# Performance work log

Hardware: AMD Instinct MI355X
Metric: run time of the kernel (lower is better)

## Reference

```python
import jax, jax.numpy as jnp
import numpy as np

B, C, H, W = 16, 64, 128, 128
HX, HY = 64, 64


def _rnn_scan(x, Wih, Whh, bih, bhh):
    """Vanilla tanh RNN, batch_first. x: [N, T, Cin] -> [N, T, Hh]."""
    # precompute input projection with one big GEMM
    pre = jnp.einsum('ntc,hc->nth', x, Wih) + bih + bhh  # [N,T,Hh]
    N = x.shape[0]
    h0 = jnp.zeros((N, Whh.shape[0]), dtype=x.dtype)

    def step(h, p):
        h = jnp.tanh(p + h @ Whh.T)
        return h, h

    _, ys = jax.lax.scan(step, h0, jnp.swapaxes(pre, 0, 1))  # [T,N,Hh]
    return jnp.swapaxes(ys, 0, 1)


def setup_inputs() -> dict:
    key = jax.random.key(0)
    ks = jax.random.split(key, 9)
    sx = 1.0 / np.sqrt(HX)
    sy = 1.0 / np.sqrt(HY)
    return {
        'x': jax.random.normal(ks[0], (B, C, H, W), dtype=jnp.float32),
        'Wih_x': jax.random.uniform(ks[1], (HX, C), jnp.float32, -sx, sx),
        'Whh_x': jax.random.uniform(ks[2], (HX, HX), jnp.float32, -sx, sx),
        'bih_x': jax.random.uniform(ks[3], (HX,), jnp.float32, -sx, sx),
        'bhh_x': jax.random.uniform(ks[4], (HX,), jnp.float32, -sx, sx),
        'Wih_y': jax.random.uniform(ks[5], (HY, HX), jnp.float32, -sy, sy),
        'Whh_y': jax.random.uniform(ks[6], (HY, HY), jnp.float32, -sy, sy),
        'bih_y': jax.random.uniform(ks[7], (HY,), jnp.float32, -sy, sy),
        'bhh_y': jax.random.uniform(ks[8], (HY,), jnp.float32, -sy, sy),
    }


def reference(x, Wih_x, Whh_x, bih_x, bhh_x, Wih_y, Whh_y, bih_y, bhh_y):
    b, c, h, w = x.shape
    # X-axis RNN: scan along width, sequences are rows
    xw = jnp.transpose(x, (0, 2, 3, 1)).reshape(b * h, w, c)  # [B*H, W, C]
    out_x = _rnn_scan(xw, Wih_x, Whh_x, bih_x, bhh_x)          # [B*H, W, HX]
    # Y-axis RNN: scan along height, sequences are columns
    xy = out_x.reshape(b, h, w, HX)
    xy = jnp.transpose(xy, (0, 2, 1, 3)).reshape(b * w, h, HX)  # [B*W, H, HX]
    out_y = _rnn_scan(xy, Wih_y, Whh_y, bih_y, bhh_y)           # [B*W, H, HY]
    out = out_y.reshape(b, w, h, HY)
    return jnp.transpose(out, (0, 3, 2, 1))  # [B, HY, H, W]
```

## Files before the change

### kernel.cpp

```cpp
#include <hip/hip_runtime.h>
#include <stdint.h>


#define TLEN 128
#define NSEQ 2048
#define PSH (NSEQ*64)
#define GT 16

typedef __bf16   bf16x8 __attribute__((ext_vector_type(8)));
typedef _Float16 f16x4  __attribute__((ext_vector_type(4)));
typedef float    f32x4  __attribute__((ext_vector_type(4)));
typedef unsigned short u16x4 __attribute__((ext_vector_type(4)));

static __device__ __forceinline__ unsigned int fbits(float f){
    union { float f; unsigned int u; } v; v.f = f; return v.u;
}
static __device__ __forceinline__ float ubits(unsigned int u){
    union { unsigned int u; float f; } v; v.u = u; return v.f;
}
static __device__ __forceinline__ float bf2f(unsigned short s){ return ubits(((unsigned int)s) << 16); }
static __device__ __forceinline__ unsigned short f2bf(float f){
    unsigned int u = fbits(f);
    return (unsigned short)((u + 0x7FFFu + ((u >> 16) & 1u)) >> 16);
}
static __device__ __forceinline__ __bf16 us2b(unsigned short s){
    union { unsigned short u; __bf16 b; } v; v.u = s; return v.b;
}
struct bfpair { __bf16 hi, lo; };
static __device__ __forceinline__ bfpair splitf(float f){
    unsigned short h = f2bf(f);
    bfpair r; r.hi = us2b(h); r.lo = us2b(f2bf(f - bf2f(h))); return r;
}
static __device__ __forceinline__ float fast_tanh(float x){
    float e = __builtin_amdgcn_exp2f(x * 2.8853900817779268f);
    return 1.0f - 2.0f * __builtin_amdgcn_rcpf(e + 1.0f);
}

__global__ __launch_bounds__(256) void k_proj0(const float* __restrict__ A,
                                               const float* __restrict__ Wih,
                                               const float* __restrict__ b1,
                                               const float* __restrict__ b2,
                                               _Float16* __restrict__ pre){
    int lane = threadIdx.x & 63;
    int wv   = threadIdx.x >> 6;
    int q    = lane >> 4, l15 = lane & 15;

    bf16x8 Whi[4][2], Wlo[4][2];
#pragma unroll
    for (int n = 0; n < 4; n++)
#pragma unroll
        for (int kc = 0; kc < 2; kc++){
            const float* p = Wih + (n * 16 + l15) * 64 + kc * 32 + q * 8;
#pragma unroll
            for (int i = 0; i < 8; i++){
                bfpair s = splitf(p[i]);
                Whi[n][kc][i] = s.hi; Wlo[n][kc][i] = s.lo;
            }
        }
    float bias[4];
#pragma unroll
    for (int n = 0; n < 4; n++){
        int j = n * 16 + l15;
        bias[n] = b1[j] + b2[j];
    }

    int row0 = blockIdx.x * 128 + wv * 32;

    float av[2][2][8];
#pragma unroll
    for (int mi = 0; mi < 2; mi++){
        int r = row0 + mi * 16 + l15;
        int b = r >> 14, hw = r & 16383;
        const float* xb = A + (size_t)b * 1048576 + hw;
#pragma unroll
        for (int kc = 0; kc < 2; kc++)
#pragma unroll
            for (int i = 0; i < 8; i++)
                av[mi][kc][i] = xb[(size_t)(kc * 32 + q * 8 + i) * 16384];
    }

#pragma unroll
    for (int mi = 0; mi < 2; mi++){
        int rb = row0 + mi * 16;
        bf16x8 Ahi[2], Alo[2];
#pragma unroll
        for (int kc = 0; kc < 2; kc++)
#pragma unroll
            for (int i = 0; i < 8; i++){
                bfpair s = splitf(av[mi][kc][i]);
                Ahi[kc][i] = s.hi; Alo[kc][i] = s.lo;
            }
        f32x4 acc[4];
#pragma unroll
        for (int n = 0; n < 4; n++) acc[n] = (f32x4){bias[n], bias[n], bias[n], bias[n]};
#pragma unroll
        for (int n = 0; n < 4; n++)
#pragma unroll
            for (int kc = 0; kc < 2; kc++){
                acc[n] = __builtin_amdgcn_mfma_f32_16x16x32_bf16(Ahi[kc], Whi[n][kc], acc[n], 0, 0, 0);
                acc[n] = __builtin_amdgcn_mfma_f32_16x16x32_bf16(Alo[kc], Whi[n][kc], acc[n], 0, 0, 0);
                acc[n] = __builtin_amdgcn_mfma_f32_16x16x32_bf16(Ahi[kc], Wlo[n][kc], acc[n], 0, 0, 0);
            }
        int bT = rb >> 14, hT = (rb >> 7) & 127, wBase = rb & 127;
        size_t seqOff = (size_t)bT * 128 + hT;
#pragma unroll
        for (int n = 0; n < 4; n++)
#pragma unroll
            for (int rr = 0; rr < 4; rr++){
                int w = wBase + q * 4 + rr;
                pre[((size_t)w * NSEQ + seqOff) * 64 + n * 16 + l15] = (_Float16)acc[n][rr];
            }
    }
}

template<int PASS>
__global__ __launch_bounds__(256) void k_scan(const _Float16* __restrict__ pre,
                                              const float* __restrict__ Whh,
                                              const float* __restrict__ Wy,
                                              const float* __restrict__ by1,
                                              const float* __restrict__ by2,
                                              _Float16* __restrict__ prey,
                                              float* __restrict__ outf){
    __shared__ alignas(16) unsigned short hbuf[2][2][16][64];
    int lane = threadIdx.x & 63;
    int wv   = threadIdx.x >> 6;
    int q = lane >> 4, l15 = lane & 15;
    int n0 = blockIdx.x * 16;
    int j0 = wv * 16 + q * 4;

    bf16x8 Ahi[2], Alo[2];
#pragma unroll
    for (int kc = 0; kc < 2; kc++){
        const float* p = Whh + (wv * 16 + l15) * 64 + kc * 32 + q * 8;
#pragma unroll
        for (int i = 0; i < 8; i++){
            bfpair s = splitf(p[i]);
            Ahi[kc][i] = s.hi; Alo[kc][i] = s.lo;
        }
    }
    bf16x8 Yhi[2], Ylo[2];
    f32x4  biasy = (f32x4){0.f, 0.f, 0.f, 0.f};
    if constexpr (PASS == 0){
#pragma unroll
        for (int kc = 0; kc < 2; kc++){
            const float* p = Wy + (wv * 16 + l15) * 64 + kc * 32 + q * 8;
#pragma unroll
            for (int i = 0; i < 8; i++){
                bfpair s = splitf(p[i]);
                Yhi[kc][i] = s.hi; Ylo[kc][i] = s.lo;
            }
        }
#pragma unroll
        for (int r = 0; r < 4; r++) biasy[r] = by1[j0 + r] + by2[j0 + r];
    }

    bf16x8 Bhi[2], Blo[2];
#pragma unroll
    for (int kc = 0; kc < 2; kc++)
#pragma unroll
        for (int i = 0; i < 8; i++){ Bhi[kc][i] = us2b(0); Blo[kc][i] = us2b(0); }

    int bb = n0 >> 7, low7 = n0 & 127;

    const _Float16* pb = pre + (size_t)(n0 + l15) * 64 + j0;
    size_t spy = (size_t)(low7 + l15) * NSEQ + (size_t)bb * 128;

    int e   = l15 & 7;
    int wj  = (((j0 >> 3) ^ e) << 3) | (j0 & 7);
    int rj0 = ((q)     ^ e) << 3;
    int rj1 = ((4 + q) ^ e) << 3;

    f16x4 ps[GT];
    u16x4 prey_st[GT];
    f32x4 outst[GT];

    for (int g = 0; g < TLEN / GT; g++){
        int G = g * GT;
#pragma unroll
        for (int u = 0; u < GT; u++)
            ps[u] = *(const f16x4*)(pb + (size_t)(G + u) * PSH);

#pragma unroll
        for (int u = 0; u < GT; u++){
            int t = G + u;
            if constexpr (PASS == 0){
                f32x4 y0 = biasy;
                f32x4 y1 = (f32x4){0.f, 0.f, 0.f, 0.f};
                y0 = __builtin_amdgcn_mfma_f32_16x16x32_bf16(Yhi[0], Bhi[0], y0, 0, 0, 0);
                y0 = __builtin_amdgcn_mfma_f32_16x16x32_bf16(Yhi[1], Bhi[1], y0, 0, 0, 0);
                y1 = __builtin_amdgcn_mfma_f32_16x16x32_bf16(Ylo[0], Bhi[0], y1, 0, 0, 0);
                y1 = __builtin_amdgcn_mfma_f32_16x16x32_bf16(Ylo[1], Bhi[1], y1, 0, 0, 0);
                y1 = __builtin_amdgcn_mfma_f32_16x16x32_bf16(Yhi[0], Blo[0], y1, 0, 0, 0);
                y1 = __builtin_amdgcn_mfma_f32_16x16x32_bf16(Yhi[1], Blo[1], y1, 0, 0, 0);
                f32x4 ys = y0 + y1;
#pragma unroll
                for (int r = 0; r < 4; r++){
                    union { _Float16 h; unsigned short s; } c;
                    c.h = (_Float16)ys[r];
                    prey_st[u][r] = c.s;
                }
            }
            f32x4 a0 = (f32x4){(float)ps[u][0], (float)ps[u][1], (float)ps[u][2], (float)ps[u][3]};
            f32x4 a1 = (f32x4){0.f, 0.f, 0.f, 0.f};
            f32x4 a2 = (f32x4){0.f, 0.f, 0.f, 0.f};
            a0 = __builtin_amdgcn_mfma_f32_16x16x32_bf16(Ahi[0], Bhi[0], a0, 0, 0, 0);
            a1 = __builtin_amdgcn_mfma_f32_16x16x32_bf16(Ahi[0], Blo[0], a1, 0, 0, 0);
            a2 = __builtin_amdgcn_mfma_f32_16x16x32_bf16(Alo[0], Bhi[0], a2, 0, 0, 0);
            a0 = __builtin_amdgcn_mfma_f32_16x16x32_bf16(Ahi[1], Bhi[1], a0, 0, 0, 0);
            a1 = __builtin_amdgcn_mfma_f32_16x16x32_bf16(Ahi[1], Blo[1], a1, 0, 0, 0);
            a2 = __builtin_amdgcn_mfma_f32_16x16x32_bf16(Alo[1], Bhi[1], a2, 0, 0, 0);
            f32x4 acc = (a0 + a1) + a2;

            u16x4 hi4, lo4;
#pragma unroll
            for (int r = 0; r < 4; r++){
                float tv = fast_tanh(acc[r]);
                if constexpr (PASS == 1) outst[u][r] = tv;
                unsigned int ub = fbits(tv);
                hi4[r] = (unsigned short)(ub >> 16);
                float lof = tv - ubits(ub & 0xFFFF0000u);
                lo4[r] = (unsigned short)(fbits(lof) >> 16);
            }
            int par = t & 1;
            *(u16x4*)&hbuf[par][0][l15][wj] = hi4;
            *(u16x4*)&hbuf[par][1][l15][wj] = lo4;
            __syncthreads();
            Bhi[0] = *(const bf16x8*)&hbuf[par][0][l15][rj0];
            Blo[0] = *(const bf16x8*)&hbuf[par][1][l15][rj0];
            Bhi[1] = *(const bf16x8*)&hbuf[par][0][l15][rj1];
            Blo[1] = *(const bf16x8*)&hbuf[par][1][l15][rj1];
        }
        if constexpr (PASS == 0){
#pragma unroll
            for (int u = 0; u < GT; u++){
                int tp = G - 1 + u;
                if (tp >= 0)
                    *(u16x4*)(prey + (spy + tp) * 64 + j0) = prey_st[u];
            }
        } else {
#pragma unroll
            for (int u = 0; u < GT; u++)
#pragma unroll
                for (int r = 0; r < 4; r++)
                    outf[((size_t)(bb * 64 + j0 + r) * TLEN + (G + u)) * 128 + low7 + l15] = outst[u][r];
        }
    }
    if constexpr (PASS == 0){
        f32x4 y0 = biasy;
        f32x4 y1 = (f32x4){0.f, 0.f, 0.f, 0.f};
        y0 = __builtin_amdgcn_mfma_f32_16x16x32_bf16(Yhi[0], Bhi[0], y0, 0, 0, 0);
        y0 = __builtin_amdgcn_mfma_f32_16x16x32_bf16(Yhi[1], Bhi[1], y0, 0, 0, 0);
        y1 = __builtin_amdgcn_mfma_f32_16x16x32_bf16(Ylo[0], Bhi[0], y1, 0, 0, 0);
        y1 = __builtin_amdgcn_mfma_f32_16x16x32_bf16(Ylo[1], Bhi[1], y1, 0, 0, 0);
        y1 = __builtin_amdgcn_mfma_f32_16x16x32_bf16(Yhi[0], Blo[0], y1, 0, 0, 0);
        y1 = __builtin_amdgcn_mfma_f32_16x16x32_bf16(Yhi[1], Blo[1], y1, 0, 0, 0);
        f32x4 ys = y0 + y1;
        u16x4 pv;
#pragma unroll
        for (int r = 0; r < 4; r++){
            union { _Float16 h; unsigned short s; } c;
            c.h = (_Float16)ys[r];
            pv[r] = c.s;
        }
        *(u16x4*)(prey + (spy + (TLEN - 1)) * 64 + j0) = pv;
    }
}

extern "C" void kernel_launch(void* const* d_in, const int* in_sizes, int n_in,
                              void* d_out, int out_size, void* d_ws, size_t ws_size,
                              hipStream_t stream){
    (void)in_sizes; (void)n_in; (void)out_size; (void)ws_size;
    const float* x    = (const float*)d_in[0];
    const float* Wihx = (const float*)d_in[1];
    const float* Whhx = (const float*)d_in[2];
    const float* bihx = (const float*)d_in[3];
    const float* bhhx = (const float*)d_in[4];
    const float* Wihy = (const float*)d_in[5];
    const float* Whhy = (const float*)d_in[6];
    const float* bihy = (const float*)d_in[7];
    const float* bhhy = (const float*)d_in[8];
    _Float16* prex = (_Float16*)d_ws;
    _Float16* prey = prex + (size_t)NSEQ * TLEN * 64;
    float* of = (float*)d_out;

    k_proj0 <<<2048, 256, 0, stream>>>(x, Wihx, bihx, bhhx, prex);
    k_scan<0><<<128, 256, 0, stream>>>(prex, Whhx, Wihy, bihy, bhhy, prey, nullptr);
    k_scan<1><<<128, 256, 0, stream>>>(prey, Whhy, nullptr, nullptr, nullptr, nullptr, of);
}
```

Before: 259.8 us.

## Interleave two sequence chunks per block in recurrent scan to hide latency

Each scan block now handles 32 sequences as two independent 16-sequence chunks. Their MFMA chains and tanh are interleaved within each timestep, sharing one barrier per step, and the grid is halved. The group size for prefetching preactivations is reduced to limit register pressure. The aim is to fill the latency of the serial dependency chain with independent work, at the cost of using fewer CUs and more registers.

```diff
diff --git a/kernel.cpp b/kernel.cpp
--- a/kernel.cpp
+++ b/kernel.cpp
@@ -5,7 +5,7 @@
 #define TLEN 128
 #define NSEQ 2048
 #define PSH (NSEQ*64)
-#define GT 16
+#define GT 8
 
 typedef __bf16   bf16x8 __attribute__((ext_vector_type(8)));
 typedef _Float16 f16x4  __attribute__((ext_vector_type(4)));
@@ -121,11 +121,11 @@
                                               const float* __restrict__ by2,
                                               _Float16* __restrict__ prey,
                                               float* __restrict__ outf){
-    __shared__ alignas(16) unsigned short hbuf[2][2][16][64];
+    __shared__ alignas(16) unsigned short hbuf[2][2][2][16][64];
     int lane = threadIdx.x & 63;
     int wv   = threadIdx.x >> 6;
     int q = lane >> 4, l15 = lane & 15;
-    int n0 = blockIdx.x * 16;
+    int n0 = blockIdx.x * 32;
     int j0 = wv * 16 + q * 4;
 
     bf16x8 Ahi[2], Alo[2];
@@ -154,115 +154,139 @@
         for (int r = 0; r < 4; r++) biasy[r] = by1[j0 + r] + by2[j0 + r];
     }
 
-    bf16x8 Bhi[2], Blo[2];
-#pragma unroll
-    for (int kc = 0; kc < 2; kc++)
-#pragma unroll
-        for (int i = 0; i < 8; i++){ Bhi[kc][i] = us2b(0); Blo[kc][i] = us2b(0); }
+    bf16x8 Bhi[2][2], Blo[2][2];
+#pragma unroll
+    for (int c = 0; c < 2; c++)
+#pragma unroll
+        for (int kc = 0; kc < 2; kc++)
+#pragma unroll
+            for (int i = 0; i < 8; i++){ Bhi[c][kc][i] = us2b(0); Blo[c][kc][i] = us2b(0); }
 
     int bb = n0 >> 7, low7 = n0 & 127;
 
-    const _Float16* pb = pre + (size_t)(n0 + l15) * 64 + j0;
-    size_t spy = (size_t)(low7 + l15) * NSEQ + (size_t)bb * 128;
+    const _Float16* pb[2];
+    size_t spy[2];
+#pragma unroll
+    for (int c = 0; c < 2; c++){
+        pb[c]  = pre + (size_t)(n0 + c * 16 + l15) * 64 + j0;
+        spy[c] = (size_t)(low7 + c * 16 + l15) * NSEQ + (size_t)bb * 128;
+    }
 
     int e   = l15 & 7;
     int wj  = (((j0 >> 3) ^ e) << 3) | (j0 & 7);
     int rj0 = ((q)     ^ e) << 3;
     int rj1 = ((4 + q) ^ e) << 3;
 
-    f16x4 ps[GT];
-    u16x4 prey_st[GT];
-    f32x4 outst[GT];
+    f16x4 ps[2][GT];
+    u16x4 prey_st[2][GT];
+    f32x4 outst[2][GT];
 
     for (int g = 0; g < TLEN / GT; g++){
         int G = g * GT;
 #pragma unroll
-        for (int u = 0; u < GT; u++)
-            ps[u] = *(const f16x4*)(pb + (size_t)(G + u) * PSH);
+        for (int c = 0; c < 2; c++)
+#pragma unroll
+            for (int u = 0; u < GT; u++)
+                ps[c][u] = *(const f16x4*)(pb[c] + (size_t)(G + u) * PSH);
 
 #pragma unroll
         for (int u = 0; u < GT; u++){
             int t = G + u;
-            if constexpr (PASS == 0){
-                f32x4 y0 = biasy;
-                f32x4 y1 = (f32x4){0.f, 0.f, 0.f, 0.f};
-                y0 = __builtin_amdgcn_mfma_f32_16x16x32_bf16(Yhi[0], Bhi[0], y0, 0, 0, 0);
-                y0 = __builtin_amdgcn_mfma_f32_16x16x32_bf16(Yhi[1], Bhi[1], y0, 0, 0, 0);
-                y1 = __builtin_amdgcn_mfma_f32_16x16x32_bf16(Ylo[0], Bhi[0], y1, 0, 0, 0);
-                y1 = __builtin_amdgcn_mfma_f32_16x16x32_bf16(Ylo[1], Bhi[1], y1, 0, 0, 0);
-                y1 = __builtin_amdgcn_mfma_f32_16x16x32_bf16(Yhi[0], Blo[0], y1, 0, 0, 0);
-                y1 = __builtin_amdgcn_mfma_f32_16x16x32_bf16(Yhi[1], Blo[1], y1, 0, 0, 0);
-                f32x4 ys = y0 + y1;
+            int par = t & 1;
+#pragma unroll
+            for (int c = 0; c < 2; c++){
+                f32x4 a0 = (f32x4){(float)ps[c][u][0], (float)ps[c][u][1],
+                                   (float)ps[c][u][2], (float)ps[c][u][3]};
+                f32x4 a1 = (f32x4){0.f, 0.f, 0.f, 0.f};
+                f32x4 a2 = (f32x4){0.f, 0.f, 0.f, 0.f};
+                a0 = __builtin_amdgcn_mfma_f32_16x16x32_bf16(Ahi[0], Bhi[c][0], a0, 0, 0, 0);
+                a1 = __builtin_amdgcn_mfma_f32_16x16x32_bf16(Ahi[0], Blo[c][0], a1, 0, 0, 0);
+                a2 = __builtin_amdgcn_mfma_f32_16x16x32_bf16(Alo[0], Bhi[c][0], a2, 0, 0, 0);
+                a0 = __builtin_amdgcn_mfma_f32_16x16x32_bf16(Ahi[1], Bhi[c][1], a0, 0, 0, 0);
+                a1 = __builtin_amdgcn_mfma_f32_16x16x32_bf16(Ahi[1], Blo[c][1], a1, 0, 0, 0);
+                a2 = __builtin_amdgcn_mfma_f32_16x16x32_bf16(Alo[1], Bhi[c][1], a2, 0, 0, 0);
+                if constexpr (PASS == 0){
+                    f32x4 y0 = biasy;
+                    f32x4 y1 = (f32x4){0.f, 0.f, 0.f, 0.f};
+                    y0 = __builtin_amdgcn_mfma_f32_16x16x32_bf16(Yhi[0], Bhi[c][0], y0, 0, 0, 0);
+                    y0 = __builtin_amdgcn_mfma_f32_16x16x32_bf16(Yhi[1], Bhi[c][1], y0, 0, 0, 0);
+                    y1 = __builtin_amdgcn_mfma_f32_16x16x32_bf16(Ylo[0], Bhi[c][0], y1, 0, 0, 0);
+                    y1 = __builtin_amdgcn_mfma_f32_16x16x32_bf16(Ylo[1], Bhi[c][1], y1, 0, 0, 0);
+                    y1 = __builtin_amdgcn_mfma_f32_16x16x32_bf16(Yhi[0], Blo[c][0], y1, 0, 0, 0);
+                    y1 = __builtin_amdgcn_mfma_f32_16x16x32_bf16(Yhi[1], Blo[c][1], y1, 0, 0, 0);
+                    f32x4 ys = y0 + y1;
+#pragma unroll
+                    for (int r = 0; r < 4; r++){
+                        union { _Float16 h; unsigned short s; } cv;
+                        cv.h = (_Float16)ys[r];
+                        prey_st[c][u][r] = cv.s;
+                    }
+                }
+                f32x4 acc = (a0 + a1) + a2;
+
+                u16x4 hi4, lo4;
 #pragma unroll
                 for (int r = 0; r < 4; r++){
-                    union { _Float16 h; unsigned short s; } c;
-                    c.h = (_Float16)ys[r];
-                    prey_st[u][r] = c.s;
+                    float tv = fast_tanh(acc[r]);
+                    if constexpr (PASS == 1) outst[c][u][r] = tv;
+                    unsigned int ub = fbits(tv);
+                    hi4[r] = (unsigned short)(ub >> 16);
+                    float lof = tv - ubits(ub & 0xFFFF0000u);
+                    lo4[r] = (unsigned short)(fbits(lof) >> 16);
                 }
-            }
-            f32x4 a0 = (f32x4){(float)ps[u][0], (float)ps[u][1], (float)ps[u][2], (float)ps[u][3]};
-            f32x4 a1 = (f32x4){0.f, 0.f, 0.f, 0.f};
-            f32x4 a2 = (f32x4){0.f, 0.f, 0.f, 0.f};
-            a0 = __builtin_amdgcn_mfma_f32_16x16x32_bf16(Ahi[0], Bhi[0], a0, 0, 0, 0);
-            a1 = __builtin_amdgcn_mfma_f32_16x16x32_bf16(Ahi[0], Blo[0], a1, 0, 0, 0);
-            a2 = __builtin_amdgcn_mfma_f32_16x16x32_bf16(Alo[0], Bhi[0], a2, 0, 0, 0);
-            a0 = __builtin_amdgcn_mfma_f32_16x16x32_bf16(Ahi[1], Bhi[1], a0, 0, 0, 0);
-            a1 = __builtin_amdgcn_mfma_f32_16x16x32_bf16(Ahi[1], Blo[1], a1, 0, 0, 0);
-            a2 = __builtin_amdgcn_mfma_f32_16x16x32_bf16(Alo[1], Bhi[1], a2, 0, 0, 0);
-            f32x4 acc = (a0 + a1) + a2;
-
-            u16x4 hi4, lo4;
+                *(u16x4*)&hbuf[c][par][0][l15][wj] = hi4;
+                *(u16x4*)&hbuf[c][par][1][l15][wj] = lo4;
+            }
+            __syncthreads();
+#pragma unroll
+            for (int c = 0; c < 2; c++){
+                Bhi[c][0] = *(const bf16x8*)&hbuf[c][par][0][l15][rj0];
+                Blo[c][0] = *(const bf16x8*)&hbuf[c][par][1][l15][rj0];
+                Bhi[c][1] = *(const bf16x8*)&hbuf[c][par][0][l15][rj1];
+                Blo[c][1] = *(const bf16x8*)&hbuf[c][par][1][l15][rj1];
+            }
+        }
+        if constexpr (PASS == 0){
+#pragma unroll
+            for (int c = 0; c < 2; c++)
+#pragma unroll
+                for (int u = 0; u < GT; u++){
+                    int tp = G - 1 + u;
+                    if (tp >= 0)
+                        *(u16x4*)(prey + (spy[c] + tp) * 64 + j0) = prey_st[c][u];
+                }
+        } else {
+#pragma unroll
+            for (int c = 0; c < 2; c++)
+#pragma unroll
+                for (int u = 0; u < GT; u++)
+#pragma unroll
+                    for (int r = 0; r < 4; r++)
+                        outf[((size_t)(bb * 64 + j0 + r) * TLEN + (G + u)) * 128
+                             + low7 + c * 16 + l15] = outst[c][u][r];
+        }
+    }
+    if constexpr (PASS == 0){
+#pragma unroll
+        for (int c = 0; c < 2; c++){
+            f32x4 y0 = biasy;
+            f32x4 y1 = (f32x4){0.f, 0.f, 0.f, 0.f};
+            y0 = __builtin_amdgcn_mfma_f32_16x16x32_bf16(Yhi[0], Bhi[c][0], y0, 0, 0, 0);
+            y0 = __builtin_amdgcn_mfma_f32_16x16x32_bf16(Yhi[1], Bhi[c][1], y0, 0, 0, 0);
+            y1 = __builtin_amdgcn_mfma_f32_16x16x32_bf16(Ylo[0], Bhi[c][0], y1, 0, 0, 0);
+            y1 = __builtin_amdgcn_mfma_f32_16x16x32_bf16(Ylo[1], Bhi[c][1], y1, 0, 0, 0);
+            y1 = __builtin_amdgcn_mfma_f32_16x16x32_bf16(Yhi[0], Blo[c][0], y1, 0, 0, 0);
+            y1 = __builtin_amdgcn_mfma_f32_16x16x32_bf16(Yhi[1], Blo[c][1], y1, 0, 0, 0);
+            f32x4 ys = y0 + y1;
+            u16x4 pv;
 #pragma unroll
             for (int r = 0; r < 4; r++){
-                float tv = fast_tanh(acc[r]);
-                if constexpr (PASS == 1) outst[u][r] = tv;
-                unsigned int ub = fbits(tv);
-                hi4[r] = (unsigned short)(ub >> 16);
-                float lof = tv - ubits(ub & 0xFFFF0000u);
-                lo4[r] = (unsigned short)(fbits(lof) >> 16);
-            }
-            int par = t & 1;
-            *(u16x4*)&hbuf[par][0][l15][wj] = hi4;
-            *(u16x4*)&hbuf[par][1][l15][wj] = lo4;
-            __syncthreads();
-            Bhi[0] = *(const bf16x8*)&hbuf[par][0][l15][rj0];
-            Blo[0] = *(const bf16x8*)&hbuf[par][1][l15][rj0];
-            Bhi[1] = *(const bf16x8*)&hbuf[par][0][l15][rj1];
-            Blo[1] = *(const bf16x8*)&hbuf[par][1][l15][rj1];
-        }
-        if constexpr (PASS == 0){
-#pragma unroll
-            for (int u = 0; u < GT; u++){
-                int tp = G - 1 + u;
-                if (tp >= 0)
-                    *(u16x4*)(prey + (spy + tp) * 64 + j0) = prey_st[u];
-            }
-        } else {
-#pragma unroll
-            for (int u = 0; u < GT; u++)
-#pragma unroll
-                for (int r = 0; r < 4; r++)
-                    outf[((size_t)(bb * 64 + j0 + r) * TLEN + (G + u)) * 128 + low7 + l15] = outst[u][r];
-        }
-    }
-    if constexpr (PASS == 0){
-        f32x4 y0 = biasy;
-        f32x4 y1 = (f32x4){0.f, 0.f, 0.f, 0.f};
-        y0 = __builtin_amdgcn_mfma_f32_16x16x32_bf16(Yhi[0], Bhi[0], y0, 0, 0, 0);
-        y0 = __builtin_amdgcn_mfma_f32_16x16x32_bf16(Yhi[1], Bhi[1], y0, 0, 0, 0);
-        y1 = __builtin_amdgcn_mfma_f32_16x16x32_bf16(Ylo[0], Bhi[0], y1, 0, 0, 0);
-        y1 = __builtin_amdgcn_mfma_f32_16x16x32_bf16(Ylo[1], Bhi[1], y1, 0, 0, 0);
-        y1 = __builtin_amdgcn_mfma_f32_16x16x32_bf16(Yhi[0], Blo[0], y1, 0, 0, 0);
-        y1 = __builtin_amdgcn_mfma_f32_16x16x32_bf16(Yhi[1], Blo[1], y1, 0, 0, 0);
-        f32x4 ys = y0 + y1;
-        u16x4 pv;
-#pragma unroll
-        for (int r = 0; r < 4; r++){
-            union { _Float16 h; unsigned short s; } c;
-            c.h = (_Float16)ys[r];
-            pv[r] = c.s;
-        }
-        *(u16x4*)(prey + (spy + (TLEN - 1)) * 64 + j0) = pv;
+                union { _Float16 h; unsigned short s; } cv;
+                cv.h = (_Float16)ys[r];
+                pv[r] = cv.s;
+            }
+            *(u16x4*)(prey + (spy[c] + (TLEN - 1)) * 64 + j0) = pv;
+        }
     }
 }
 
@@ -284,6 +308,6 @@
     float* of = (float*)d_out;
 
     k_proj0 <<<2048, 256, 0, stream>>>(x, Wihx, bihx, bhhx, prex);
-    k_scan<0><<<128, 256, 0, stream>>>(prex, Whhx, Wihy, bihy, bhhy, prey, nullptr);
-    k_scan<1><<<128, 256, 0, stream>>>(prey, Whhy, nullptr, nullptr, nullptr, nullptr, of);
-}
+    k_scan<0><<<64, 256, 0, stream>>>(prex, Whhx, Wihy, bihy, bhhy, prey, nullptr);
+    k_scan<1><<<64, 256, 0, stream>>>(prey, Whhy, nullptr, nullptr, nullptr, nullptr, of);
+}
```

After: 353.9 us. +36.2%, slower.
